# Optimization experiments

Hardware: AMD Instinct MI355X
Metric: run time of the kernel (lower is better)

Reference implementation:

```python
import jax, jax.numpy as jnp
import numpy as np
from jax import lax

N, H, W = 8, 64, 64
SX1, SX2, THX, TLX = 256, 256, 256, 256
E1, E2, A1, OT = 256, 64, 128, 256
EBD = SX2 // 2            # ebd_factor=2
TXC = THX + TLX           # 512
IN1 = SX1 + TXC           # 768
BV = EBD + TXC            # 640


def upsample2x_align_corners(x):
    # bilinear, align_corners=True, scale_factor=2 (matches nn.Upsample)
    n, c, h, w = x.shape
    ho, wo = 2 * h, 2 * w
    ys = jnp.linspace(0.0, h - 1.0, ho)
    xs = jnp.linspace(0.0, w - 1.0, wo)
    y0 = jnp.floor(ys).astype(jnp.int32); y1 = jnp.minimum(y0 + 1, h - 1)
    x0 = jnp.floor(xs).astype(jnp.int32); x1 = jnp.minimum(x0 + 1, w - 1)
    wy = (ys - y0).astype(x.dtype); wx = (xs - x0).astype(x.dtype)
    xh = x[:, :, y0, :] * (1.0 - wy)[None, None, :, None] + x[:, :, y1, :] * wy[None, None, :, None]
    return xh[:, :, :, x0] * (1.0 - wx) + xh[:, :, :, x1] * wx


def conv1x1(x, w, b=None):
    # x: [N,C,H,W], w: [O,C]
    y = jnp.einsum('nchw,oc->nohw', x, w)
    if b is not None:
        y = y + b[None, :, None, None]
    return y


def conv3x3(x, w, b):
    y = lax.conv_general_dilated(x, w, window_strides=(1, 1), padding=((1, 1), (1, 1)),
                                 dimension_numbers=('NCHW', 'OIHW', 'NCHW'))
    return y + b[None, :, None, None]


def setup_inputs() -> dict:
    key = jax.random.key(0)
    ks = jax.random.split(key, 20)
    g = lambda k, shape, fan: jax.random.normal(k, shape, jnp.float32) * np.sqrt(2.0 / fan)
    return {
        'sx1': jax.random.normal(ks[0], (N, SX1, H, W), jnp.float32),
        'sx2': jax.random.normal(ks[1], (N, SX2, H, W), jnp.float32),
        't_hx': jax.random.normal(ks[2], (N, THX, H, W), jnp.float32),
        'tx': jax.random.normal(ks[3], (N, TLX, H // 2, W // 2), jnp.float32),
        'W_t1': g(ks[4], (E1, IN1), IN1 + E1), 'b_t1': jnp.zeros((E1,), jnp.float32),
        'W_t2': g(ks[5], (E2, E1), E1 + E2),
        'W_t3': g(ks[6], (SX2, E2), E2 + SX2),
        'W_U': g(ks[7], (SX2, SX2), 2 * SX2), 'b_U': jnp.zeros((SX2,), jnp.float32),
        'W_V': g(ks[8], (EBD, SX2), SX2 + EBD), 'b_V': jnp.zeros((EBD,), jnp.float32),
        'W_a1': g(ks[9], (A1, BV), BV + A1), 'b_a1': jnp.zeros((A1,), jnp.float32),
        'W_a2': g(ks[10], (BV, A1), A1 + BV), 'b_a2': jnp.zeros((BV,), jnp.float32),
        'W_ot': g(ks[11], (OT, BV, 3, 3), 9 * (BV + OT)), 'b_ot': jnp.zeros((OT,), jnp.float32),
    }


def reference(sx1, sx2, t_hx, tx, W_t1, b_t1, W_t2, W_t3, W_U, b_U, W_V, b_V,
              W_a1, b_a1, W_a2, b_a2, W_ot, b_ot):
    tx_up = upsample2x_align_corners(tx)
    txc = jnp.concatenate([t_hx, tx_up], axis=1)          # [N,TXC,H,W]
    st = jnp.concatenate([sx1, txc], axis=1)              # [N,IN1,H,W]
    w = jax.nn.relu(conv1x1(st, W_t1, b_t1))
    w = jnp.mean(w, axis=(2, 3), keepdims=True)           # GAP -> [N,E1,1,1]
    w = jax.nn.relu(conv1x1(w, W_t2))
    w = conv1x1(w, W_t3)                                  # [N,SX2,1,1]
    norm = jnp.sqrt(jnp.sum(w * w, axis=1, keepdims=True))
    w = w / jnp.maximum(norm, 1e-12)                      # F.normalize(dim=1)
    b = jax.nn.relu(conv1x1(sx2, W_U, b_U))
    b = b * w                                             # AdaptiveConv2d grouped 1x1 == per-sample per-channel scale
    b = jax.nn.relu(conv1x1(b, W_V, b_V))
    b = jnp.concatenate([b, txc], axis=1)                 # [N,BV,H,W]
    a = jax.nn.relu(conv1x1(b, W_a1, b_a1))
    a = jax.nn.sigmoid(conv1x1(a, W_a2, b_a2))
    a = a * b
    a = jax.nn.relu(conv3x3(a, W_ot, b_ot))               # [N,OT,H,W]
    return (a, w)
```

## Files before the change

kernel.cpp:

```cpp
#include <hip/hip_runtime.h>
#include <hip/hip_bf16.h>

#define PP 4096
#define HH 64
#define WW 64

typedef __attribute__((ext_vector_type(8))) short short8b;
typedef __attribute__((ext_vector_type(4))) float f32x4;

static __device__ __forceinline__ float bf2f(short s) {
    union { unsigned int u; float f; } cv; cv.u = ((unsigned int)(unsigned short)s) << 16; return cv.f;
}
static __device__ __forceinline__ short f2bf(float f) {
    __hip_bfloat16 h = __float2bfloat16(f);
    return *reinterpret_cast<short*>(&h);
}

static __device__ __forceinline__ void pack16(const float* __restrict__ W,
                                              short* __restrict__ dst,
                                              int MT, int K, int s) {
    int total = MT * 2 * (K / 64) * 64;
    if (s >= total) return;
    int lane = s & 63;
    int rest = s >> 6;
    int ks = rest & 1; rest >>= 1;
    int mt = rest % MT;
    int cc = rest / MT;
    int o   = mt * 16 + (lane & 15);
    int ch0 = cc * 64 + ks * 32 + (lane >> 4) * 8;
    short8b v;
    #pragma unroll
    for (int j = 0; j < 8; ++j) v[j] = f2bf(W[(size_t)o * K + ch0 + j]);
    ((short8b*)dst)[s] = v;
}

__global__ void k_packall(const float* __restrict__ Wt1, const float* __restrict__ WU,
                          const float* __restrict__ WV, const float* __restrict__ Wa1,
                          const float* __restrict__ Wa2, const float* __restrict__ Wot,
                          short* __restrict__ Wt1p, short* __restrict__ WUp,
                          short* __restrict__ WVp, short* __restrict__ Wa1p,
                          short* __restrict__ Wa2p, short* __restrict__ Wotp) {
    int b = blockIdx.x, tid = threadIdx.x;
    if (b < 96)       { pack16(Wt1, Wt1p, 16, 768, (b)       * 256 + tid); }
    else if (b < 128) { pack16(WU,  WUp,  16, 256, (b - 96)  * 256 + tid); }
    else if (b < 144) { pack16(WV,  WVp,   8, 256, (b - 128) * 256 + tid); }
    else if (b < 184) { pack16(Wa1, Wa1p,  8, 640, (b - 144) * 256 + tid); }
    else if (b < 224) { pack16(Wa2, Wa2p, 40, 128, (b - 184) * 256 + tid); }
    else {
        int s = (b - 224) * 256 + tid;
        int lane = s & 63;
        int rest = s >> 6;
        int ks = rest & 1;  rest >>= 1;
        int mt = rest & 15; rest >>= 4;
        int cc = rest % 10;
        int k9 = rest / 10;
        int o   = mt * 16 + (lane & 15);
        int ch0 = cc * 64 + ks * 32 + (lane >> 4) * 8;
        short8b v{};
        #pragma unroll
        for (int j = 0; j < 8; ++j)
            v[j] = f2bf(Wot[((size_t)o * 640 + ch0 + j) * 9 + k9]);
        ((short8b*)Wotp)[s] = v;
    }
}

__global__ void k_t2h_all(const float* __restrict__ t_hx, const float* __restrict__ tx,
                          short* __restrict__ txc, short* __restrict__ txh) {
    __shared__ short T[64 * 65];
    int tid = threadIdx.x;
    int by = blockIdx.y;
    const float* src; short* dst; int P, pitch, yb;
    if (by < 4)  { src = t_hx; dst = txc; P = 4096; pitch = 512; yb = by; }
    else { if (blockIdx.x >= 16) return;
           src = tx;   dst = txh; P = 1024; pitch = 256; yb = by - 4; }
    int p0 = blockIdx.x * 64, c0 = yb * 64, n = blockIdx.z;
    #pragma unroll
    for (int it = 0; it < 16; ++it) {
        int slot = it * 256 + tid;
        int ch = slot >> 6, px = slot & 63;
        T[ch * 65 + px] = f2bf(src[((size_t)(n * 256 + c0 + ch)) * P + p0 + px]);
    }
    __syncthreads();
    #pragma unroll
    for (int it = 0; it < 16; ++it) {
        int slot = it * 256 + tid;
        int px = slot >> 6, ch = slot & 63;
        dst[((size_t)n * P + p0 + px) * pitch + c0 + ch] = T[ch * 65 + px];
    }
}

__global__ void k_up(const short* __restrict__ txh, short* __restrict__ txc) {
    int tid = threadIdx.x;
    int cg = tid & 31, pxl = tid >> 5;
    int px = blockIdx.x * 8 + pxl;
    int n  = blockIdx.z;
    int y = px >> 6, x = px & 63;
    const float s = 31.0f / 63.0f;
    float fy = y * s, fx = x * s;
    int y0 = (int)fy, x0 = (int)fx;
    int y1 = min(y0 + 1, 31), x1 = min(x0 + 1, 31);
    float wy = fy - (float)y0, wx = fx - (float)x0;
    const short8b* base = (const short8b*)(txh + ((size_t)n * 1024) * 256);
    short8b a = base[((size_t)(y0 * 32 + x0) * 256 + cg * 8) >> 3];
    short8b b = base[((size_t)(y0 * 32 + x1) * 256 + cg * 8) >> 3];
    short8b c = base[((size_t)(y1 * 32 + x0) * 256 + cg * 8) >> 3];
    short8b d = base[((size_t)(y1 * 32 + x1) * 256 + cg * 8) >> 3];
    short8b r;
    #pragma unroll
    for (int j = 0; j < 8; ++j) {
        float v = (bf2f(a[j]) * (1.f - wy) + bf2f(c[j]) * wy) * (1.f - wx)
                + (bf2f(b[j]) * (1.f - wy) + bf2f(d[j]) * wy) * wx;
        r[j] = f2bf(v);
    }
    *(short8b*)(txc + ((size_t)n * PP + px) * 512 + 256 + cg * 8) = r;
}

static __device__ __forceinline__ void stage64(const short* __restrict__ src, int pitch,
                                               int c0, size_t rowbase, short* lds, int tid) {
    #pragma unroll
    for (int it = 0; it < 4; ++it) {
        int idx = it * 256 + tid;
        int px = idx >> 3, cg = idx & 7;
        short8b v = *(const short8b*)(src + (rowbase + px) * (size_t)pitch + c0 + cg * 8);
        int elem = (px * 64 + cg * 8) ^ ((px & 7) << 3);
        *(short8b*)&lds[elem] = v;
    }
}
static __device__ __forceinline__ void stage64f(const float* __restrict__ ten, int C,
                                                int c0, int n, int pxbase,
                                                short* lds, int tid) {
    int chp = tid & 31;
    int pxg = tid >> 5;
    const float* p0 = ten + ((size_t)(n * C + c0 + chp * 2)) * PP + pxbase + pxg * 16;
    const float* p1 = p0 + PP;
    #pragma unroll
    for (int kq = 0; kq < 4; ++kq) {
        f32x4 a = *(const f32x4*)(p0 + kq * 4);
        f32x4 b = *(const f32x4*)(p1 + kq * 4);
        #pragma unroll
        for (int j = 0; j < 4; ++j) {
            int px = pxg * 16 + kq * 4 + j;
            int idx = px * 64 + ((chp * 2) ^ ((px & 7) << 3));
            unsigned int u = (unsigned int)(unsigned short)f2bf(a[j])
                           | ((unsigned int)(unsigned short)f2bf(b[j]) << 16);
            *(unsigned int*)&lds[idx] = u;
        }
    }
}
static __device__ __forceinline__ short8b afrag(const short* lds, int pw, int mf, int ks, int lane) {
    int px = pw * 64 + mf * 16 + (lane & 15);
    int elem = (px * 64 + ks * 32 + ((lane >> 4) * 8)) ^ ((px & 7) << 3);
    return *(const short8b*)&lds[elem];
}
#define GEMM_PROLOG \
    int tid = threadIdx.x, lane = tid & 63, wid = tid >> 6; \
    int pw = wid & 1, ow = wid >> 1; \
    int bx = blockIdx.x, pt = blockIdx.y, n = blockIdx.z; \
    size_t rowbase = (size_t)n * PP + pt * 128; \
    f32x4 acc[4][4] = {}; (void)bx; (void)rowbase;
#define GEMM_STEP(MT) { \
    short8b afr[4][2], bfr[4][2]; \
    _Pragma("unroll") for (int mf = 0; mf < 4; ++mf) \
        _Pragma("unroll") for (int ks = 0; ks < 2; ++ks) afr[mf][ks] = afrag(lds, pw, mf, ks, lane); \
    _Pragma("unroll") for (int nf = 0; nf < 4; ++nf) { \
        int mt_g = bx * 8 + ow * 4 + nf; \
        _Pragma("unroll") for (int ks = 0; ks < 2; ++ks) \
            bfr[nf][ks] = wfv[(((size_t)cc * (MT) + mt_g) * 2 + ks) * 64 + lane]; } \
    _Pragma("unroll") for (int ks = 0; ks < 2; ++ks) \
        _Pragma("unroll") for (int mf = 0; mf < 4; ++mf) \
            _Pragma("unroll") for (int nf = 0; nf < 4; ++nf) \
                acc[mf][nf] = __builtin_amdgcn_mfma_f32_16x16x32_bf16(afr[mf][ks], bfr[nf][ks], acc[mf][nf], 0, 0, 0); }

__global__ __launch_bounds__(256) void k_gemm_gap(const float* __restrict__ sx1,
        const short* __restrict__ txc, const short* __restrict__ wf,
        const float* __restrict__ bias, float* __restrict__ part) {
    __shared__ short lds[128 * 64];
    __shared__ float red[128 * 2];
    GEMM_PROLOG
    const short8b* wfv = (const short8b*)wf;
    for (int cc = 0; cc < 12; ++cc) {
        __syncthreads();
        if (cc < 4) stage64f(sx1, 256, cc * 64, n, pt * 128, lds, tid);
        else        stage64(txc, 512, (cc - 4) * 64, rowbase, lds, tid);
        __syncthreads();
        GEMM_STEP(16)
    }
    #pragma unroll
    for (int nf = 0; nf < 4; ++nf) {
        int o = bx * 128 + ow * 64 + nf * 16 + (lane & 15);
        float b = bias[o];
        float s = 0.f;
        #pragma unroll
        for (int mf = 0; mf < 4; ++mf)
            #pragma unroll
            for (int r = 0; r < 4; ++r) {
                float v = acc[mf][nf][r] + b;
                s += v > 0.f ? v : 0.f;
            }
        s += __shfl_xor(s, 16);
        s += __shfl_xor(s, 32);
        if (lane < 16) red[(ow * 64 + nf * 16 + lane) * 2 + pw] = s;
    }
    __syncthreads();
    if (tid < 128)
        part[((size_t)n * 256 + bx * 128 + tid) * 32 + pt] = red[tid * 2] + red[tid * 2 + 1];
}

__global__ __launch_bounds__(256) void k_gemm_bU(const float* __restrict__ sx2,
        const short* __restrict__ wf, const float* __restrict__ bias,
        const float* __restrict__ wvec, short* __restrict__ bUh) {
    __shared__ short lds[128 * 64];
    GEMM_PROLOG
    const short8b* wfv = (const short8b*)wf;
    for (int cc = 0; cc < 4; ++cc) {
        __syncthreads();
        stage64f(sx2, 256, cc * 64, n, pt * 128, lds, tid);
        __syncthreads();
        GEMM_STEP(16)
    }
    #pragma unroll
    for (int nf = 0; nf < 4; ++nf) {
        int o = bx * 128 + ow * 64 + nf * 16 + (lane & 15);
        float b = bias[o], wv = wvec[n * 256 + o];
        #pragma unroll
        for (int mf = 0; mf < 4; ++mf)
            #pragma unroll
            for (int r = 0; r < 4; ++r) {
                int px = pw * 64 + mf * 16 + (lane >> 4) * 4 + r;
                float v = acc[mf][nf][r] + b;
                v = v > 0.f ? v : 0.f;
                bUh[(rowbase + px) * 256 + o] = f2bf(v * wv);
            }
    }
}

__global__ __launch_bounds__(256) void k_gemm_bV(const short* __restrict__ bUh,
        const short* __restrict__ wf, const float* __restrict__ bias,
        short* __restrict__ bVh) {
    __shared__ short lds[128 * 64];
    GEMM_PROLOG
    const short8b* wfv = (const short8b*)wf;
    for (int cc = 0; cc < 4; ++cc) {
        __syncthreads();
        stage64(bUh, 256, cc * 64, rowbase, lds, tid);
        __syncthreads();
        GEMM_STEP(8)
    }
    #pragma unroll
    for (int nf = 0; nf < 4; ++nf) {
        int o = ow * 64 + nf * 16 + (lane & 15);
        float b = bias[o];
        #pragma unroll
        for (int mf = 0; mf < 4; ++mf)
            #pragma unroll
            for (int r = 0; r < 4; ++r) {
                int px = pw * 64 + mf * 16 + (lane >> 4) * 4 + r;
                float v = acc[mf][nf][r] + b;
                bVh[(rowbase + px) * 128 + o] = f2bf(v > 0.f ? v : 0.f);
            }
    }
}

__global__ __launch_bounds__(256) void k_gemm_a1(const short* __restrict__ bVh,
        const short* __restrict__ txc, const short* __restrict__ wf,
        const float* __restrict__ bias, short* __restrict__ a1h) {
    __shared__ short lds[128 * 64];
    GEMM_PROLOG
    const short8b* wfv = (const short8b*)wf;
    for (int cc = 0; cc < 10; ++cc) {
        __syncthreads();
        if (cc < 2) stage64(bVh, 128, cc * 64, rowbase, lds, tid);
        else        stage64(txc, 512, (cc - 2) * 64, rowbase, lds, tid);
        __syncthreads();
        GEMM_STEP(8)
    }
    #pragma unroll
    for (int nf = 0; nf < 4; ++nf) {
        int o = ow * 64 + nf * 16 + (lane & 15);
        float b = bias[o];
        #pragma unroll
        for (int mf = 0; mf < 4; ++mf)
            #pragma unroll
            for (int r = 0; r < 4; ++r) {
                int px = pw * 64 + mf * 16 + (lane >> 4) * 4 + r;
                float v = acc[mf][nf][r] + b;
                a1h[(rowbase + px) * 128 + o] = f2bf(v > 0.f ? v : 0.f);
            }
    }
}

__global__ __launch_bounds__(256) void k_gemm_amul(const short* __restrict__ a1h,
        const short* __restrict__ wf, const float* __restrict__ bias,
        const short* __restrict__ bVh, const short* __restrict__ txc,
        short* __restrict__ amulH) {
    __shared__ short lds[128 * 64];
    GEMM_PROLOG
    const short8b* wfv = (const short8b*)wf;
    for (int cc = 0; cc < 2; ++cc) {
        __syncthreads();
        stage64(a1h, 128, cc * 64, rowbase, lds, tid);
        __syncthreads();
        GEMM_STEP(40)
    }
    #pragma unroll
    for (int nf = 0; nf < 4; ++nf) {
        int o = bx * 128 + ow * 64 + nf * 16 + (lane & 15);
        float b = bias[o];
        #pragma unroll
        for (int mf = 0; mf < 4; ++mf)
            #pragma unroll
            for (int r = 0; r < 4; ++r) {
                int px = pw * 64 + mf * 16 + (lane >> 4) * 4 + r;
                float xv = acc[mf][nf][r] + b;
                float sg = 1.0f / (1.0f + expf(-xv));
                float bval = (o < 128) ? bf2f(bVh[(rowbase + px) * 128 + o])
                                       : bf2f(txc[(rowbase + px) * 512 + o - 128]);
                amulH[(rowbase + px) * 640 + o] = f2bf(sg * bval);
            }
    }
}

__global__ void k_wvec(const float* __restrict__ part, const float* __restrict__ Wt2,
                       const float* __restrict__ Wt3, float* __restrict__ wvec,
                       float* __restrict__ out_w) {
    int n = blockIdx.x, tid = threadIdx.x;
    __shared__ float sm1[256];
    __shared__ float sm2[64];
    __shared__ float smr[4];
    float s = 0.0f;
    #pragma unroll
    for (int t = 0; t < 32; ++t) s += part[(size_t)(n * 256 + tid) * 32 + t];
    sm1[tid] = s * (1.0f / 4096.0f);
    __syncthreads();
    if (tid < 64) {
        float a = 0.0f;
        for (int c = 0; c < 256; ++c) a = fmaf(Wt2[tid * 256 + c], sm1[c], a);
        sm2[tid] = a > 0.0f ? a : 0.0f;
    }
    __syncthreads();
    float w3 = 0.0f;
    for (int e = 0; e < 64; ++e) w3 = fmaf(Wt3[tid * 64 + e], sm2[e], w3);
    float q = w3 * w3;
    int lane = tid & 63, wv = tid >> 6;
    #pragma unroll
    for (int off = 32; off > 0; off >>= 1) q += __shfl_down(q, off);
    if (lane == 0) smr[wv] = q;
    __syncthreads();
    float nrm = sqrtf(smr[0] + smr[1] + smr[2] + smr[3]);
    nrm = fmaxf(nrm, 1e-12f);
    float w = w3 / nrm;
    wvec[n * 256 + tid] = w;
    out_w[n * 256 + tid] = w;
}

#define WLOAD(dst, u, kss) { \
    _Pragma("unroll") for (int mf = 0; mf < 4; ++mf) { \
        int mt_g = bx * 8 + mw * 4 + mf; \
        dst[mf] = wf[(((size_t)(u) * 16 + mt_g) * 2 + (kss)) * 64 + lane]; } }

#define BLOAD(dst, kyv, kxv, ksv) { \
    _Pragma("unroll") for (int nf = 0; nf < 4; ++nf) { \
        int col = nf * 16 + (lane & 15); \
        int chc = col + (kxv); \
        int row_eff = nw + (kyv); \
        int elem = ((row_eff * 66 + chc) * 64 + (ksv) * 32 + (lane >> 4) * 8) \
                   ^ ((chc & 7) << 3); \
        dst[nf] = *(const short8b*)&lds_x[elem]; } }

#define MFMA16(W, B) { \
    _Pragma("unroll") for (int mf = 0; mf < 4; ++mf) \
        _Pragma("unroll") for (int nf = 0; nf < 4; ++nf) \
            acc[mf][nf] = __builtin_amdgcn_mfma_f32_16x16x32_bf16( \
                W[mf], B[nf], acc[mf][nf], 0, 0, 0); }

__global__ __launch_bounds__(512, 1) void k_conv3_mfma(
        const short* __restrict__ amulH, const short* __restrict__ Wfrag,
        const float* __restrict__ bot, float* __restrict__ out_a) {
    __shared__ short lds_x[6 * 66 * 64];
    const int tid  = threadIdx.x;
    const int lane = tid & 63;
    const int wid  = tid >> 6;
    const int mw = wid & 1;
    const int nw = wid >> 1;
    const int qx = blockIdx.x;
    const int bx = blockIdx.y;
    const int n  = blockIdx.z;

    f32x4 acc[4][4] = {};
    const short8b* wf = (const short8b*)Wfrag;

    const int scol = tid >> 3, scg = tid & 7;
    short8b vreg[6];
    #pragma unroll
    for (int it = 0; it < 6; ++it) {
        int gr = qx * 4 - 1 + it;
        short8b t{};
        if (gr >= 0 && gr < 64)
            t = *(const short8b*)(amulH + ((size_t)(n * PP + gr * 64 + scol)) * 640 + scg * 8);
        vreg[it] = t;
    }
    if (tid < 96) {
        int rr = tid >> 4, side = (tid >> 3) & 1, cg = tid & 7;
        int chc = side ? 65 : 0;
        int elem = ((rr * 66 + chc) * 64 + cg * 8) ^ ((chc & 7) << 3);
        *(short8b*)&lds_x[elem] = short8b{};
    }

    short8b wA[4], wB[4], bfrA[4], bfrB[4];
    WLOAD(wA, 0, 0)

    for (int cc = 0; cc < 10; ++cc) {
        __syncthreads();
        {
            int chc = scol + 1;
            #pragma unroll
            for (int it = 0; it < 6; ++it) {
                int elem = ((it * 66 + chc) * 64 + scg * 8) ^ ((chc & 7) << 3);
                *(short8b*)&lds_x[elem] = vreg[it];
            }
        }
        __syncthreads();
        if (cc < 9) {
            #pragma unroll
            for (int it = 0; it < 6; ++it) {
                int gr = qx * 4 - 1 + it;
                short8b t{};
                if (gr >= 0 && gr < 64)
                    t = *(const short8b*)(amulH + ((size_t)(n * PP + gr * 64 + scol)) * 640
                                          + (cc + 1) * 64 + scg * 8);
                vreg[it] = t;
            }
        }
        BLOAD(bfrA, 0, 0, 0)
        #pragma unroll
        for (int h = 0; h < 18; ++h) {
            const bool even = ((h & 1) == 0);
            if (h < 17) {
                const int hn = h + 1;
                const int k9n = hn >> 1, ksn = hn & 1;
                const int kyn = k9n / 3, kxn = k9n % 3;
                const int un = k9n * 10 + cc;
                if (even) { BLOAD(bfrB, kyn, kxn, ksn) WLOAD(wB, un, ksn) }
                else      { BLOAD(bfrA, kyn, kxn, ksn) WLOAD(wA, un, ksn) }
            } else {
                WLOAD(wA, cc + 1, 0)
            }
            if (even) { MFMA16(wA, bfrA) } else { MFMA16(wB, bfrB) }
        }
    }
    #pragma unroll
    for (int mf = 0; mf < 4; ++mf) {
        int o = bx * 128 + mw * 64 + mf * 16 + (lane >> 4) * 4;
        #pragma unroll
        for (int r = 0; r < 4; ++r) {
            float bias = bot[o + r];
            #pragma unroll
            for (int nf = 0; nf < 4; ++nf) {
                int p = qx * 256 + nw * 64 + nf * 16 + (lane & 15);
                float v = acc[mf][nf][r] + bias;
                out_a[((size_t)(n * 256 + o + r)) * PP + p] = v > 0.f ? v : 0.f;
            }
        }
    }
}

extern "C" void kernel_launch(void* const* d_in, const int* in_sizes, int n_in,
                              void* d_out, int out_size, void* d_ws, size_t ws_size,
                              hipStream_t stream) {
    static const int want[18] = {
        8388608, 8388608, 8388608, 2097152, 196608, 256, 16384, 16384,
        65536, 256, 32768, 128, 81920, 128, 81920, 640, 1474560, 256
    };
    const void* ptr[18];
    bool used[64];
    for (int i = 0; i < 64; ++i) used[i] = false;
    bool ok = (n_in >= 18 && n_in <= 64);
    for (int k = 0; k < 18 && ok; ++k) {
        ptr[k] = nullptr;
        for (int i = 0; i < n_in; ++i) {
            if (!used[i] && in_sizes[i] == want[k]) { ptr[k] = d_in[i]; used[i] = true; break; }
        }
        if (!ptr[k]) ok = false;
    }
    if (!ok) { for (int k = 0; k < 18; ++k) ptr[k] = d_in[k]; }

    const float* sx1  = (const float*)ptr[0];
    const float* sx2  = (const float*)ptr[1];
    const float* t_hx = (const float*)ptr[2];
    const float* tx   = (const float*)ptr[3];
    const float* Wt1  = (const float*)ptr[4];
    const float* bt1  = (const float*)ptr[5];
    const float* Wt2  = (const float*)ptr[6];
    const float* Wt3  = (const float*)ptr[7];
    const float* WU   = (const float*)ptr[8];
    const float* bU   = (const float*)ptr[9];
    const float* WV   = (const float*)ptr[10];
    const float* bV   = (const float*)ptr[11];
    const float* Wa1  = (const float*)ptr[12];
    const float* ba1  = (const float*)ptr[13];
    const float* Wa2  = (const float*)ptr[14];
    const float* ba2  = (const float*)ptr[15];
    const float* Wot  = (const float*)ptr[16];
    const float* bot  = (const float*)ptr[17];

    char* base = (char*)d_ws;
    short* txc   = (short*)base;
    short* bUh   = (short*)(base + (size_t)33554432);
    short* amulH = (short*)(base + (size_t)33554432);
    short* txh   = (short*)(base + (size_t)75497472);
    short* bVh   = (short*)(base + (size_t)75497472);
    short* a1h   = (short*)(base + (size_t)83886080);
    float* part  = (float*)(base + (size_t)92274688);
    float* wvec  = (float*)(base + (size_t)92536832);
    short* Wt1p  = (short*)(base + (size_t)92545024);
    short* WUp   = (short*)(base + (size_t)92938240);
    short* WVp   = (short*)(base + (size_t)93069312);
    short* Wa1p  = (short*)(base + (size_t)93134848);
    short* Wa2p  = (short*)(base + (size_t)93298688);
    short* Wotp  = (short*)(base + (size_t)93462528);

    float* out_a = (float*)d_out;
    float* out_w = out_a + (size_t)8 * 256 * PP;

    k_packall<<<dim3(944), 256, 0, stream>>>(Wt1, WU, WV, Wa1, Wa2, Wot,
                                             Wt1p, WUp, WVp, Wa1p, Wa2p, Wotp);
    k_t2h_all<<<dim3(64, 8, 8), 256, 0, stream>>>(t_hx, tx, txc, txh);
    k_up<<<dim3(512, 1, 8), 256, 0, stream>>>(txh, txc);

    k_gemm_gap <<<dim3(2, 32, 8), 256, 0, stream>>>(sx1, txc, Wt1p, bt1, part);
    k_wvec     <<<dim3(8),        256, 0, stream>>>(part, Wt2, Wt3, wvec, out_w);
    k_gemm_bU  <<<dim3(2, 32, 8), 256, 0, stream>>>(sx2, WUp, bU, wvec, bUh);
    k_gemm_bV  <<<dim3(1, 32, 8), 256, 0, stream>>>(bUh, WVp, bV, bVh);
    k_gemm_a1  <<<dim3(1, 32, 8), 256, 0, stream>>>(bVh, txc, Wa1p, ba1, a1h);
    k_gemm_amul<<<dim3(5, 32, 8), 256, 0, stream>>>(a1h, Wa2p, ba2, bVh, txc, amulH);
    k_conv3_mfma<<<dim3(16, 2, 8), 512, 0, stream>>>(amulH, Wotp, bot, out_a);
}
```

Before: 272.3 us.

## Split conv3x3 K-halves across waves, double per-wave pixel tile, reduce via LDS

The 3x3 conv MFMA kernel now gives each wave one of the two 32-channel K sub-slices and two output rows (8 N-fragments) instead of one row with both K sub-slices. Each weight fragment is therefore reused across twice as many B fragments, and the weight loads per wave are halved. Partial sums from the ks=1 waves are then reduced into the ks=0 waves through LDS in four segments before bias and ReLU. The accumulator doubles to 32 f32x4 registers per wave, which raises register pressure, and the reduction adds extra barriers and LDS traffic.

```diff
diff --git a/kernel.cpp b/kernel.cpp
--- a/kernel.cpp
+++ b/kernel.cpp
@@ -358,18 +358,17 @@
         int mt_g = bx * 8 + mw * 4 + mf; \
         dst[mf] = wf[(((size_t)(u) * 16 + mt_g) * 2 + (kss)) * 64 + lane]; } }
 
-#define BLOAD(dst, kyv, kxv, ksv) { \
-    _Pragma("unroll") for (int nf = 0; nf < 4; ++nf) { \
-        int col = nf * 16 + (lane & 15); \
-        int chc = col + (kxv); \
-        int row_eff = nw + (kyv); \
-        int elem = ((row_eff * 66 + chc) * 64 + (ksv) * 32 + (lane >> 4) * 8) \
+#define BLOAD8(dst, kyv, kxv) { \
+    _Pragma("unroll") for (int nf = 0; nf < 8; ++nf) { \
+        int chc = (nf & 3) * 16 + (lane & 15) + (kxv); \
+        int row_eff = rp * 2 + (nf >> 2) + (kyv); \
+        int elem = ((row_eff * 66 + chc) * 64 + ks * 32 + (lane >> 4) * 8) \
                    ^ ((chc & 7) << 3); \
         dst[nf] = *(const short8b*)&lds_x[elem]; } }
 
-#define MFMA16(W, B) { \
+#define MFMA32(W, B) { \
     _Pragma("unroll") for (int mf = 0; mf < 4; ++mf) \
-        _Pragma("unroll") for (int nf = 0; nf < 4; ++nf) \
+        _Pragma("unroll") for (int nf = 0; nf < 8; ++nf) \
             acc[mf][nf] = __builtin_amdgcn_mfma_f32_16x16x32_bf16( \
                 W[mf], B[nf], acc[mf][nf], 0, 0, 0); }
 
@@ -381,12 +380,13 @@
     const int lane = tid & 63;
     const int wid  = tid >> 6;
     const int mw = wid & 1;
-    const int nw = wid >> 1;
+    const int rp = (wid >> 1) & 1;
+    const int ks = wid >> 2;
     const int qx = blockIdx.x;
     const int bx = blockIdx.y;
     const int n  = blockIdx.z;
 
-    f32x4 acc[4][4] = {};
+    f32x4 acc[4][8] = {};
     const short8b* wf = (const short8b*)Wfrag;
 
     const int scol = tid >> 3, scg = tid & 7;
@@ -406,8 +406,8 @@
         *(short8b*)&lds_x[elem] = short8b{};
     }
 
-    short8b wA[4], wB[4], bfrA[4], bfrB[4];
-    WLOAD(wA, 0, 0)
+    short8b wA[4], wB[4], bfr[8];
+    WLOAD(wA, 0, ks)
 
     for (int cc = 0; cc < 10; ++cc) {
         __syncthreads();
@@ -431,34 +431,46 @@
                 vreg[it] = t;
             }
         }
-        BLOAD(bfrA, 0, 0, 0)
-        #pragma unroll
-        for (int h = 0; h < 18; ++h) {
-            const bool even = ((h & 1) == 0);
-            if (h < 17) {
-                const int hn = h + 1;
-                const int k9n = hn >> 1, ksn = hn & 1;
-                const int kyn = k9n / 3, kxn = k9n % 3;
-                const int un = k9n * 10 + cc;
-                if (even) { BLOAD(bfrB, kyn, kxn, ksn) WLOAD(wB, un, ksn) }
-                else      { BLOAD(bfrA, kyn, kxn, ksn) WLOAD(wA, un, ksn) }
+        #pragma unroll
+        for (int t9 = 0; t9 < 9; ++t9) {
+            const int ky = t9 / 3, kx = t9 % 3;
+            const bool even = ((t9 & 1) == 0);
+            if (t9 < 8) {
+                const int un = (t9 + 1) * 10 + cc;
+                if (even) { WLOAD(wB, un, ks) } else { WLOAD(wA, un, ks) }
             } else {
-                WLOAD(wA, cc + 1, 0)
-            }
-            if (even) { MFMA16(wA, bfrA) } else { MFMA16(wB, bfrB) }
-        }
-    }
-    #pragma unroll
-    for (int mf = 0; mf < 4; ++mf) {
-        int o = bx * 128 + mw * 64 + mf * 16 + (lane >> 4) * 4;
-        #pragma unroll
-        for (int r = 0; r < 4; ++r) {
-            float bias = bot[o + r];
-            #pragma unroll
-            for (int nf = 0; nf < 4; ++nf) {
-                int p = qx * 256 + nw * 64 + nf * 16 + (lane & 15);
-                float v = acc[mf][nf][r] + bias;
-                out_a[((size_t)(n * 256 + o + r)) * PP + p] = v > 0.f ? v : 0.f;
+                WLOAD(wB, cc + 1, ks)
+            }
+            BLOAD8(bfr, ky, kx)
+            if (even) { MFMA32(wA, bfr) } else { MFMA32(wB, bfr) }
+        }
+        wA[0] = wB[0]; wA[1] = wB[1]; wA[2] = wB[2]; wA[3] = wB[3];
+    }
+    float* lf = (float*)lds_x;
+    #pragma unroll
+    for (int seg = 0; seg < 4; ++seg) {
+        __syncthreads();
+        if (ks == 1) {
+            int slot = mw + rp * 2;
+            #pragma unroll
+            for (int nf = 0; nf < 8; ++nf)
+                #pragma unroll
+                for (int r = 0; r < 4; ++r)
+                    lf[slot * 2048 + (nf * 4 + r) * 64 + lane] = acc[seg][nf][r];
+        }
+        __syncthreads();
+        if (ks == 0) {
+            int slot = mw + rp * 2;
+            int o = bx * 128 + mw * 64 + seg * 16 + (lane >> 4) * 4;
+            #pragma unroll
+            for (int r = 0; r < 4; ++r) {
+                float bias = bot[o + r];
+                #pragma unroll
+                for (int nf = 0; nf < 8; ++nf) {
+                    int p = qx * 256 + (rp * 2 + (nf >> 2)) * 64 + (nf & 3) * 16 + (lane & 15);
+                    float v = acc[seg][nf][r] + lf[slot * 2048 + (nf * 4 + r) * 64 + lane] + bias;
+                    out_a[((size_t)(n * 256 + o + r)) * PP + p] = v > 0.f ? v : 0.f;
+                }
             }
         }
     }
```

New measurement: 430.5 us. +58.1%, slower.
